# Kernel tuning notes

Hardware: AMD Instinct MI355X
Metric: run time of the kernel (lower is better)

The kernel has to match this reference:

```python
import jax, jax.numpy as jnp
import numpy as np

B, N, IN_F, OUT_F = 32, 1024, 256, 256
ALPHA = 0.2  # LeakyReLU negative slope
NEG_INF = -9e15  # matches torch's -9000000000000000.0 masking constant


def setup_inputs() -> dict:
    key = jax.random.key(0)
    k1, k2, k3, k4 = jax.random.split(key, 4)
    h = jax.random.normal(k1, (B, N, IN_F), dtype=jnp.float32)
    adj = jax.random.randint(k2, (B, N, N), 0, 2, dtype=jnp.int32)
    W = jax.random.normal(k3, (OUT_F, IN_F), dtype=jnp.float32) * 0.05
    a = jax.random.normal(k4, (1, 2 * OUT_F), dtype=jnp.float32) * 0.05
    return {"h": h, "adj": adj, "W": W, "a": a}


def reference(h, adj, W, a):
    # Wh: (B, N, out)
    Wh = jnp.einsum("bni,oi->bno", h, W)
    # Decompose a([Wh_i || Wh_j]) = Wh_i . a1 + Wh_j . a2 (identical math,
    # avoids the O(B*N^2*2*out) concat intermediate of the torch code).
    a1 = a[0, :OUT_F]   # (out,)
    a2 = a[0, OUT_F:]   # (out,)
    si = Wh @ a1        # (B, N) score contribution of source node i
    sj = Wh @ a2        # (B, N) score contribution of neighbor node j
    e = jax.nn.leaky_relu(si[:, :, None] + sj[:, None, :], negative_slope=ALPHA)
    attention = jnp.where(adj > 0, e, NEG_INF)
    attention = jax.nn.softmax(attention, axis=-1)
    # dropout omitted (eval mode)
    h_prime = jnp.einsum("bij,bjo->bio", attention, Wh)
    return jax.nn.elu(h_prime)
```

## Files before the change

### kernel.cpp

```cpp
#include <hip/hip_runtime.h>
#include <hip/hip_bf16.h>


#define ALPHA 0.2f

typedef __bf16 bf16x8 __attribute__((ext_vector_type(8)));
typedef __bf16 bf16x4 __attribute__((ext_vector_type(4)));
typedef float  f32x4  __attribute__((ext_vector_type(4)));

__global__ __launch_bounds__(256) void k1_gemm1(const float* __restrict__ h,
                                                const float* __restrict__ W,
                                                __bf16* __restrict__ whT) {
    __shared__ __bf16 hA[64 * 72];
    __shared__ __bf16 hB[256 * 72];
    const int t    = threadIdx.x;
    const int r0   = blockIdx.x * 64;
    const int b    = r0 >> 10;
    const int n0   = r0 & 1023;
    const int w    = t >> 6;
    const int l    = t & 63;
    const int ln   = l & 15;
    const int quad = l >> 4;

    f32x4 acc[4][4] = {};

    for (int kc = 0; kc < 4; ++kc) {
        const int k0 = kc * 64;
        #pragma unroll
        for (int it = 0; it < 4; ++it) {
            const int row = it * 16 + (t >> 4);
            const int seg = t & 15;
            const float4 v = *(const float4*)&h[(size_t)(r0 + row) * 256 + k0 + seg * 4];
            bf16x4 pv = {(__bf16)v.x, (__bf16)v.y, (__bf16)v.z, (__bf16)v.w};
            *(bf16x4*)&hA[row * 72 + seg * 4] = pv;
        }
        #pragma unroll
        for (int it = 0; it < 16; ++it) {
            const int o   = it * 16 + (t >> 4);
            const int seg = t & 15;
            const float4 v = *(const float4*)&W[(size_t)o * 256 + k0 + seg * 4];
            bf16x4 pv = {(__bf16)v.x, (__bf16)v.y, (__bf16)v.z, (__bf16)v.w};
            *(bf16x4*)&hB[o * 72 + seg * 4] = pv;
        }
        __syncthreads();
        #pragma unroll
        for (int kk = 0; kk < 2; ++kk) {
            bf16x8 af[4], bfr[4];
            #pragma unroll
            for (int ri = 0; ri < 4; ++ri)
                af[ri] = *(const bf16x8*)&hA[(ri * 16 + ln) * 72 + kk * 32 + quad * 8];
            #pragma unroll
            for (int oi = 0; oi < 4; ++oi)
                bfr[oi] = *(const bf16x8*)&hB[(w * 64 + oi * 16 + ln) * 72 + kk * 32 + quad * 8];
            #pragma unroll
            for (int ri = 0; ri < 4; ++ri)
                #pragma unroll
                for (int oi = 0; oi < 4; ++oi)
                    acc[ri][oi] = __builtin_amdgcn_mfma_f32_16x16x32_bf16(
                        af[ri], bfr[oi], acc[ri][oi], 0, 0, 0);
        }
        __syncthreads();
    }
    #pragma unroll
    for (int ri = 0; ri < 4; ++ri) {
        const int n = n0 + ri * 16 + quad * 4;
        #pragma unroll
        for (int oi = 0; oi < 4; ++oi) {
            const int o = w * 64 + oi * 16 + ln;
            bf16x4 pv = {(__bf16)acc[ri][oi][0], (__bf16)acc[ri][oi][1],
                         (__bf16)acc[ri][oi][2], (__bf16)acc[ri][oi][3]};
            *(bf16x4*)&whT[((size_t)b * 256 + o) * 1024 + n] = pv;
        }
    }
}

__global__ __launch_bounds__(256) void k2_scores(const __bf16* __restrict__ whT,
                                                 const float* __restrict__ a,
                                                 float* __restrict__ si,
                                                 float* __restrict__ sj) {
    const int tid = blockIdx.x * 256 + threadIdx.x;
    const int b = tid >> 10, n = tid & 1023;
    const __bf16* base = whT + (size_t)b * 256 * 1024 + n;
    float s1 = 0.f, s2 = 0.f;
    #pragma unroll 8
    for (int o = 0; o < 256; ++o) {
        const float v = (float)base[(size_t)o * 1024];
        s1 += v * a[o];
        s2 += v * a[256 + o];
    }
    si[tid] = s1;
    sj[tid] = s2;
}

__global__ __launch_bounds__(256) void k3_attn(const int* __restrict__ adj,
                                               const __bf16* __restrict__ whT,
                                               const float* __restrict__ si_g,
                                               const float* __restrict__ sj_g,
                                               float* __restrict__ out) {
    __shared__ __bf16 lds_w[256 * 72];
    __shared__ __bf16 lds_s[64 * 72];
    __shared__ float  lds_denom[64];
    const int t    = threadIdx.x;
    const int b    = blockIdx.y;
    const int i0   = blockIdx.x * 64;
    const int w    = t >> 6;
    const int l    = t & 63;
    const int ln   = l & 15;
    const int quad = l >> 4;
    const int g    = t >> 4;
    const int j4   = t & 15;

    float si_r[4];
    #pragma unroll
    for (int m = 0; m < 4; ++m) si_r[m] = si_g[b * 1024 + i0 + m * 16 + g];

    float dsum[4] = {0.f, 0.f, 0.f, 0.f};
    f32x4 acc[4][4] = {};
    const __bf16* whTb = whT + (size_t)b * 256 * 1024;

    for (int jc = 0; jc < 16; ++jc) {
        const int j0 = jc * 64;
        #pragma unroll
        for (int it = 0; it < 8; ++it) {
            const int o   = it * 32 + (t >> 3);
            const int seg = t & 7;
            const bf16x8 v = *(const bf16x8*)&whTb[(size_t)o * 1024 + j0 + seg * 8];
            *(bf16x8*)&lds_w[o * 72 + seg * 8] = v;
        }
        #pragma unroll
        for (int m = 0; m < 4; ++m) {
            const int il = m * 16 + g;
            const int i  = i0 + il;
            const int jb = j0 + j4 * 4;
            const int4   a4 = *(const int4*)&adj[((size_t)(b * 1024 + i)) * 1024 + jb];
            const float4 s4 = *(const float4*)&sj_g[b * 1024 + jb];
            float e0 = si_r[m] + s4.x; e0 = e0 > 0.f ? e0 : ALPHA * e0;
            float e1 = si_r[m] + s4.y; e1 = e1 > 0.f ? e1 : ALPHA * e1;
            float e2 = si_r[m] + s4.z; e2 = e2 > 0.f ? e2 : ALPHA * e2;
            float e3 = si_r[m] + s4.w; e3 = e3 > 0.f ? e3 : ALPHA * e3;
            const float w0 = a4.x > 0 ? __expf(e0) : 0.f;
            const float w1 = a4.y > 0 ? __expf(e1) : 0.f;
            const float w2 = a4.z > 0 ? __expf(e2) : 0.f;
            const float w3 = a4.w > 0 ? __expf(e3) : 0.f;
            bf16x4 pv = {(__bf16)w0, (__bf16)w1, (__bf16)w2, (__bf16)w3};
            dsum[m] += (float)pv[0] + (float)pv[1] + (float)pv[2] + (float)pv[3];
            *(bf16x4*)&lds_s[il * 72 + j4 * 4] = pv;
        }
        __syncthreads();
        #pragma unroll
        for (int kk = 0; kk < 2; ++kk) {
            bf16x8 af[4], bfr[4];
            #pragma unroll
            for (int ri = 0; ri < 4; ++ri)
                af[ri] = *(const bf16x8*)&lds_s[(ri * 16 + ln) * 72 + kk * 32 + quad * 8];
            #pragma unroll
            for (int oi = 0; oi < 4; ++oi)
                bfr[oi] = *(const bf16x8*)&lds_w[(w * 64 + oi * 16 + ln) * 72 + kk * 32 + quad * 8];
            #pragma unroll
            for (int ri = 0; ri < 4; ++ri)
                #pragma unroll
                for (int oi = 0; oi < 4; ++oi)
                    acc[ri][oi] = __builtin_amdgcn_mfma_f32_16x16x32_bf16(
                        af[ri], bfr[oi], acc[ri][oi], 0, 0, 0);
        }
        __syncthreads();
    }
    #pragma unroll
    for (int m = 0; m < 4; ++m) {
        float v = dsum[m];
        v += __shfl_xor(v, 1);
        v += __shfl_xor(v, 2);
        v += __shfl_xor(v, 4);
        v += __shfl_xor(v, 8);
        if (j4 == 0) lds_denom[m * 16 + g] = v;
    }
    __syncthreads();
    #pragma unroll
    for (int ri = 0; ri < 4; ++ri) {
        #pragma unroll
        for (int q = 0; q < 4; ++q) {
            const int il = ri * 16 + quad * 4 + q;
            const float dinv = 1.0f / fmaxf(lds_denom[il], 1e-30f);
            #pragma unroll
            for (int oi = 0; oi < 4; ++oi) {
                const int o = w * 64 + oi * 16 + ln;
                const float v = acc[ri][oi][q] * dinv;
                const float r = v > 0.f ? v : __expf(v) - 1.f;
                out[((size_t)(b * 1024 + i0 + il)) * 256 + o] = r;
            }
        }
    }
}

extern "C" void kernel_launch(void* const* d_in, const int* in_sizes, int n_in,
                              void* d_out, int out_size, void* d_ws, size_t ws_size,
                              hipStream_t stream) {
    const float* h   = (const float*)d_in[0];
    const int*   adj = (const int*)d_in[1];
    const float* W   = (const float*)d_in[2];
    const float* a   = (const float*)d_in[3];
    float* out = (float*)d_out;

    __bf16* whT = (__bf16*)d_ws;
    float*  si  = (float*)((char*)d_ws + (size_t)16777216);
    float*  sj  = si + 32768;

    k1_gemm1<<<512, 256, 0, stream>>>(h, W, whT);
    k2_scores<<<128, 256, 0, stream>>>(whT, a, si, sj);
    k3_attn<<<dim3(16, 32), 256, 0, stream>>>(adj, whT, si, sj, out);
}
```

Baseline: 304.6 us.

## Bit-pack adjacency, fuse score computation into GEMM, and register-prefetch tiles

Adds a pre-pass that packs the int32 adjacency matrix into 64-bit ballot masks, so the attention kernel reads one bit per edge instead of four bytes. The score kernel is merged into the first GEMM: the output tile is staged through shared memory, written out with coalesced stores, and reduced against a there. Both GEMM loops now prefetch the next tile into registers while the current one is computed. The adjacency is still read in full once by the mask kernel, and the register prefetch raises register pressure.

```diff
diff --git a/kernel.cpp b/kernel.cpp
--- a/kernel.cpp
+++ b/kernel.cpp
@@ -7,12 +7,31 @@
 typedef __bf16 bf16x8 __attribute__((ext_vector_type(8)));
 typedef __bf16 bf16x4 __attribute__((ext_vector_type(4)));
 typedef float  f32x4  __attribute__((ext_vector_type(4)));
+typedef unsigned long long u64;
+
+__global__ __launch_bounds__(256) void k0_mask(const int* __restrict__ adj,
+                                               u64* __restrict__ mask) {
+    const int wid = (blockIdx.x * 256 + threadIdx.x) >> 6;
+    const int l   = threadIdx.x & 63;
+    const size_t base = (size_t)wid * 64;
+    #pragma unroll 4
+    for (int it = 0; it < 64; ++it) {
+        const size_t word = base + it;
+        const int v = adj[word * 64 + l];
+        const u64 m = __ballot(v > 0);
+        if (l == 0) mask[word] = m;
+    }
+}
 
 __global__ __launch_bounds__(256) void k1_gemm1(const float* __restrict__ h,
                                                 const float* __restrict__ W,
-                                                __bf16* __restrict__ whT) {
+                                                const float* __restrict__ a_g,
+                                                __bf16* __restrict__ whT,
+                                                float* __restrict__ si,
+                                                float* __restrict__ sj) {
     __shared__ __bf16 hA[64 * 72];
     __shared__ __bf16 hB[256 * 72];
+    __shared__ float  red[512];
     const int t    = threadIdx.x;
     const int r0   = blockIdx.x * 64;
     const int b    = r0 >> 10;
@@ -23,26 +42,38 @@
     const int quad = l >> 4;
 
     f32x4 acc[4][4] = {};
+    float4 ha_r[4], wb_r[16];
+
+    #pragma unroll
+    for (int it = 0; it < 4; ++it)
+        ha_r[it] = *(const float4*)&h[(size_t)(r0 + it * 16 + (t >> 4)) * 256 + (t & 15) * 4];
+    #pragma unroll
+    for (int it = 0; it < 16; ++it)
+        wb_r[it] = *(const float4*)&W[(size_t)(it * 16 + (t >> 4)) * 256 + (t & 15) * 4];
 
     for (int kc = 0; kc < 4; ++kc) {
-        const int k0 = kc * 64;
         #pragma unroll
         for (int it = 0; it < 4; ++it) {
-            const int row = it * 16 + (t >> 4);
-            const int seg = t & 15;
-            const float4 v = *(const float4*)&h[(size_t)(r0 + row) * 256 + k0 + seg * 4];
+            const float4 v = ha_r[it];
             bf16x4 pv = {(__bf16)v.x, (__bf16)v.y, (__bf16)v.z, (__bf16)v.w};
-            *(bf16x4*)&hA[row * 72 + seg * 4] = pv;
+            *(bf16x4*)&hA[(it * 16 + (t >> 4)) * 72 + (t & 15) * 4] = pv;
         }
         #pragma unroll
         for (int it = 0; it < 16; ++it) {
-            const int o   = it * 16 + (t >> 4);
-            const int seg = t & 15;
-            const float4 v = *(const float4*)&W[(size_t)o * 256 + k0 + seg * 4];
+            const float4 v = wb_r[it];
             bf16x4 pv = {(__bf16)v.x, (__bf16)v.y, (__bf16)v.z, (__bf16)v.w};
-            *(bf16x4*)&hB[o * 72 + seg * 4] = pv;
-        }
-        __syncthreads();
+            *(bf16x4*)&hB[(it * 16 + (t >> 4)) * 72 + (t & 15) * 4] = pv;
+        }
+        __syncthreads();
+        if (kc < 3) {
+            const int k0 = (kc + 1) * 64;
+            #pragma unroll
+            for (int it = 0; it < 4; ++it)
+                ha_r[it] = *(const float4*)&h[(size_t)(r0 + it * 16 + (t >> 4)) * 256 + k0 + (t & 15) * 4];
+            #pragma unroll
+            for (int it = 0; it < 16; ++it)
+                wb_r[it] = *(const float4*)&W[(size_t)(it * 16 + (t >> 4)) * 256 + k0 + (t & 15) * 4];
+        }
         #pragma unroll
         for (int kk = 0; kk < 2; ++kk) {
             bf16x8 af[4], bfr[4];
@@ -61,38 +92,50 @@
         }
         __syncthreads();
     }
+
     #pragma unroll
     for (int ri = 0; ri < 4; ++ri) {
-        const int n = n0 + ri * 16 + quad * 4;
+        const int n = ri * 16 + quad * 4;
         #pragma unroll
         for (int oi = 0; oi < 4; ++oi) {
             const int o = w * 64 + oi * 16 + ln;
             bf16x4 pv = {(__bf16)acc[ri][oi][0], (__bf16)acc[ri][oi][1],
                          (__bf16)acc[ri][oi][2], (__bf16)acc[ri][oi][3]};
-            *(bf16x4*)&whT[((size_t)b * 256 + o) * 1024 + n] = pv;
-        }
-    }
-}
-
-__global__ __launch_bounds__(256) void k2_scores(const __bf16* __restrict__ whT,
-                                                 const float* __restrict__ a,
-                                                 float* __restrict__ si,
-                                                 float* __restrict__ sj) {
-    const int tid = blockIdx.x * 256 + threadIdx.x;
-    const int b = tid >> 10, n = tid & 1023;
-    const __bf16* base = whT + (size_t)b * 256 * 1024 + n;
-    float s1 = 0.f, s2 = 0.f;
-    #pragma unroll 8
-    for (int o = 0; o < 256; ++o) {
-        const float v = (float)base[(size_t)o * 1024];
-        s1 += v * a[o];
-        s2 += v * a[256 + o];
-    }
-    si[tid] = s1;
-    sj[tid] = s2;
-}
-
-__global__ __launch_bounds__(256) void k3_attn(const int* __restrict__ adj,
+            *(bf16x4*)&hB[o * 72 + n] = pv;
+        }
+    }
+    __syncthreads();
+
+    #pragma unroll
+    for (int it = 0; it < 8; ++it) {
+        const int o   = w * 64 + it * 8 + (l >> 3);
+        const int seg = l & 7;
+        const bf16x8 v = *(const bf16x8*)&hB[o * 72 + seg * 8];
+        *(bf16x8*)&whT[((size_t)b * 256 + o) * 1024 + n0 + seg * 8] = v;
+    }
+
+    {
+        float s1 = 0.f, s2 = 0.f;
+        #pragma unroll 8
+        for (int oi = 0; oi < 64; ++oi) {
+            const int o = w * 64 + oi;
+            const float v = (float)hB[o * 72 + l];
+            s1 += v * a_g[o];
+            s2 += v * a_g[256 + o];
+        }
+        red[w * 64 + l]       = s1;
+        red[256 + w * 64 + l] = s2;
+    }
+    __syncthreads();
+    if (t < 64) {
+        si[b * 1024 + n0 + t] = red[t] + red[64 + t] + red[128 + t] + red[192 + t];
+    } else if (t < 128) {
+        const int n = t - 64;
+        sj[b * 1024 + n0 + n] = red[256 + n] + red[320 + n] + red[384 + n] + red[448 + n];
+    }
+}
+
+__global__ __launch_bounds__(256) void k3_attn(const u64* __restrict__ mask,
                                                const __bf16* __restrict__ whT,
                                                const float* __restrict__ si_g,
                                                const float* __restrict__ sj_g,
@@ -116,37 +159,52 @@
 
     float dsum[4] = {0.f, 0.f, 0.f, 0.f};
     f32x4 acc[4][4] = {};
-    const __bf16* whTb = whT + (size_t)b * 256 * 1024;
+    const __bf16* whTb  = whT + (size_t)b * 256 * 1024;
+    const u64*    maskb = mask + ((size_t)b * 1024) * 16;
+
+    bf16x8 vreg[8];
+    u64    msk[4];
+    float4 sjv;
+
+    #pragma unroll
+    for (int it = 0; it < 8; ++it)
+        vreg[it] = *(const bf16x8*)&whTb[(size_t)(it * 32 + (t >> 3)) * 1024 + (t & 7) * 8];
+    #pragma unroll
+    for (int m = 0; m < 4; ++m) msk[m] = maskb[(size_t)(i0 + m * 16 + g) * 16];
+    sjv = *(const float4*)&sj_g[b * 1024 + j4 * 4];
 
     for (int jc = 0; jc < 16; ++jc) {
         const int j0 = jc * 64;
         #pragma unroll
-        for (int it = 0; it < 8; ++it) {
-            const int o   = it * 32 + (t >> 3);
-            const int seg = t & 7;
-            const bf16x8 v = *(const bf16x8*)&whTb[(size_t)o * 1024 + j0 + seg * 8];
-            *(bf16x8*)&lds_w[o * 72 + seg * 8] = v;
-        }
+        for (int it = 0; it < 8; ++it)
+            *(bf16x8*)&lds_w[(it * 32 + (t >> 3)) * 72 + (t & 7) * 8] = vreg[it];
         #pragma unroll
         for (int m = 0; m < 4; ++m) {
-            const int il = m * 16 + g;
-            const int i  = i0 + il;
-            const int jb = j0 + j4 * 4;
-            const int4   a4 = *(const int4*)&adj[((size_t)(b * 1024 + i)) * 1024 + jb];
-            const float4 s4 = *(const float4*)&sj_g[b * 1024 + jb];
-            float e0 = si_r[m] + s4.x; e0 = e0 > 0.f ? e0 : ALPHA * e0;
-            float e1 = si_r[m] + s4.y; e1 = e1 > 0.f ? e1 : ALPHA * e1;
-            float e2 = si_r[m] + s4.z; e2 = e2 > 0.f ? e2 : ALPHA * e2;
-            float e3 = si_r[m] + s4.w; e3 = e3 > 0.f ? e3 : ALPHA * e3;
-            const float w0 = a4.x > 0 ? __expf(e0) : 0.f;
-            const float w1 = a4.y > 0 ? __expf(e1) : 0.f;
-            const float w2 = a4.z > 0 ? __expf(e2) : 0.f;
-            const float w3 = a4.w > 0 ? __expf(e3) : 0.f;
+            const int il   = m * 16 + g;
+            const unsigned bits = (unsigned)(msk[m] >> (4 * j4)) & 0xFu;
+            float e0 = si_r[m] + sjv.x; e0 = e0 > 0.f ? e0 : ALPHA * e0;
+            float e1 = si_r[m] + sjv.y; e1 = e1 > 0.f ? e1 : ALPHA * e1;
+            float e2 = si_r[m] + sjv.z; e2 = e2 > 0.f ? e2 : ALPHA * e2;
+            float e3 = si_r[m] + sjv.w; e3 = e3 > 0.f ? e3 : ALPHA * e3;
+            const float w0 = (bits & 1u) ? __expf(e0) : 0.f;
+            const float w1 = (bits & 2u) ? __expf(e1) : 0.f;
+            const float w2 = (bits & 4u) ? __expf(e2) : 0.f;
+            const float w3 = (bits & 8u) ? __expf(e3) : 0.f;
             bf16x4 pv = {(__bf16)w0, (__bf16)w1, (__bf16)w2, (__bf16)w3};
             dsum[m] += (float)pv[0] + (float)pv[1] + (float)pv[2] + (float)pv[3];
             *(bf16x4*)&lds_s[il * 72 + j4 * 4] = pv;
         }
         __syncthreads();
+        if (jc < 15) {
+            const int j1 = j0 + 64;
+            #pragma unroll
+            for (int it = 0; it < 8; ++it)
+                vreg[it] = *(const bf16x8*)&whTb[(size_t)(it * 32 + (t >> 3)) * 1024 + j1 + (t & 7) * 8];
+            #pragma unroll
+            for (int m = 0; m < 4; ++m)
+                msk[m] = maskb[(size_t)(i0 + m * 16 + g) * 16 + jc + 1];
+            sjv = *(const float4*)&sj_g[b * 1024 + j1 + j4 * 4];
+        }
         #pragma unroll
         for (int kk = 0; kk < 2; ++kk) {
             bf16x8 af[4], bfr[4];
@@ -165,6 +223,7 @@
         }
         __syncthreads();
     }
+
     #pragma unroll
     for (int m = 0; m < 4; ++m) {
         float v = dsum[m];
@@ -201,11 +260,12 @@
     const float* a   = (const float*)d_in[3];
     float* out = (float*)d_out;
 
-    __bf16* whT = (__bf16*)d_ws;
-    float*  si  = (float*)((char*)d_ws + (size_t)16777216);
-    float*  sj  = si + 32768;
-
-    k1_gemm1<<<512, 256, 0, stream>>>(h, W, whT);
-    k2_scores<<<128, 256, 0, stream>>>(whT, a, si, sj);
-    k3_attn<<<dim3(16, 32), 256, 0, stream>>>(adj, whT, si, sj, out);
-}
+    __bf16* whT  = (__bf16*)d_ws;
+    float*  si   = (float*)((char*)d_ws + (size_t)16777216);
+    float*  sj   = (float*)((char*)d_ws + (size_t)16777216 + 131072);
+    u64*    mask = (u64*)((char*)d_ws + (size_t)16777216 + 262144);
+
+    k0_mask<<<2048, 256, 0, stream>>>(adj, mask);
+    k1_gemm1<<<512, 256, 0, stream>>>(h, W, a, whT, si, sj);
+    k3_attn<<<dim3(16, 32), 256, 0, stream>>>(mask, whT, si, sj, out);
+}
```

New measurement: 286.3 us. -6.0%, faster.
